# Kernel optimization log

Measured on AMD Instinct MI355X. Metric: run time of the kernel, lower is better.

Reference implementation:

```python
import jax, jax.numpy as jnp
import numpy as np

B, S, H = 2, 2048, 2048
NH, NKV, D = 32, 8, 64
GROUPS = NH // NKV
SCALE = D ** -0.5


def rotate_half(x):
    x1, x2 = x[..., : D // 2], x[..., D // 2 :]
    return jnp.concatenate((-x2, x1), axis=-1)


def setup_inputs() -> dict:
    key = jax.random.key(0)
    ks = jax.random.split(key, 8)
    x = jax.random.normal(ks[0], (B, S, H), dtype=jnp.float32)
    cos = jax.random.uniform(ks[1], (B, S, D), dtype=jnp.float32)
    sin = jax.random.uniform(ks[2], (B, S, D), dtype=jnp.float32)
    mask = jnp.tril(jnp.ones((S, S), dtype=jnp.int32))[None, None]  # causal (1,1,S,S)
    std = H ** -0.5
    wq = jax.random.normal(ks[3], (NH * D, H), dtype=jnp.float32) * std
    wk = jax.random.normal(ks[4], (NKV * D, H), dtype=jnp.float32) * std
    wv = jax.random.normal(ks[5], (NKV * D, H), dtype=jnp.float32) * std
    wo = jax.random.normal(ks[6], (H, NH * D), dtype=jnp.float32) * std
    return {"x": x, "cos": cos, "sin": sin, "mask": mask,
            "wq": wq, "wk": wk, "wv": wv, "wo": wo}


def reference(x, cos, sin, mask, wq, wk, wv, wo):
    b, s, _ = x.shape
    # projections (Linear: x @ W^T, no bias)
    q = (x @ wq.T).reshape(b, s, NH, D).transpose(0, 2, 1, 3)    # (b, nh, s, d)
    k = (x @ wk.T).reshape(b, s, NKV, D).transpose(0, 2, 1, 3)   # (b, nkv, s, d)
    v = (x @ wv.T).reshape(b, s, NKV, D).transpose(0, 2, 1, 3)
    # RoPE
    c = cos[:, None, :, :]
    sn = sin[:, None, :, :]
    q = q * c + rotate_half(q) * sn
    k = k * c + rotate_half(k) * sn
    # GQA: repeat KV heads
    k = jnp.repeat(k, GROUPS, axis=1)   # (b, nh, s, d)
    v = jnp.repeat(v, GROUPS, axis=1)
    scores = jnp.einsum("bhqd,bhkd->bhqk", q, k) * SCALE
    scores = jnp.where(mask == 0, -jnp.inf, scores)
    weights = jax.nn.softmax(scores, axis=-1)
    out = jnp.einsum("bhqk,bhkd->bhqd", weights, v)
    out = out.transpose(0, 2, 1, 3).reshape(b, s, NH * D)
    return out @ wo.T
```

## Files before the change

kernel.cpp:

```cpp
#include <hip/hip_runtime.h>
#include <hip/hip_bf16.h>
#include <math.h>

typedef __attribute__((ext_vector_type(8))) short bf16x8;
typedef __attribute__((ext_vector_type(4))) float f32x4;

__device__ __forceinline__ float bf2f(ushort u) {
  union { unsigned u; float f; } v; v.u = ((unsigned)u) << 16; return v.f;
}
__device__ __forceinline__ ushort f2bf(float f) {
  union { float f; unsigned u; } v; v.f = f;
  unsigned r = v.u + 0x7FFFu + ((v.u >> 16) & 1u);
  return (ushort)(r >> 16);
}
#if __has_builtin(__builtin_amdgcn_exp2f)
#define EXP2F(x) __builtin_amdgcn_exp2f(x)
#else
#define EXP2F(x) exp2f(x)
#endif
__device__ __forceinline__ void gl_lds16(const ushort* g, ushort* l) {
  __builtin_amdgcn_global_load_lds(
      (const __attribute__((address_space(1))) unsigned int*)g,
      (__attribute__((address_space(3))) unsigned int*)l, 16, 0, 0);
}

static const long XB   = 0;
static const long WQB  = 8388608;
static const long WKB  = 12582912;
static const long WVB  = 13631488;
static const long WOB  = 14680064;
static const long COSB = 18874368;
static const long SINB = 19136512;
static const long QB   = 19398656;
static const long KB   = 27787264;
static const long VTB  = 29884416;

__global__ void detect_dtype(const ushort* __restrict__ x, int* __restrict__ flag) {
  __shared__ int cnt;
  if (threadIdx.x == 0) cnt = 0;
  __syncthreads();
  int local = 0;
  for (int j = 0; j < 32; j++) {
    ushort u = x[threadIdx.x + j * 256];
    int e = (u >> 7) & 0xFF;
    if (e >= 100 && e <= 142) local++;
  }
  atomicAdd(&cnt, local);
  __syncthreads();
  if (threadIdx.x == 0) *flag = (cnt >= 6554) ? 1 : 0;
}

__global__ void cast_all(const void* __restrict__ s0, const void* __restrict__ s1,
                         const void* __restrict__ s2, const void* __restrict__ s3,
                         const void* __restrict__ s4, const void* __restrict__ s5,
                         const void* __restrict__ s6,
                         ushort* __restrict__ d0, ushort* __restrict__ d1,
                         ushort* __restrict__ d2, ushort* __restrict__ d3,
                         ushort* __restrict__ d4, ushort* __restrict__ d5,
                         ushort* __restrict__ d6, const int* __restrict__ flag) {
  if (*flag) return;
  const long N = 2424832;
  for (long i = (long)blockIdx.x * blockDim.x + threadIdx.x; i < N;
       i += (long)gridDim.x * blockDim.x) {
    const float4* s; ushort* d; long off;
    if      (i < 1048576) { s = (const float4*)s0; d = d0; off = i; }
    else if (i < 1572864) { s = (const float4*)s1; d = d1; off = i - 1048576; }
    else if (i < 1703936) { s = (const float4*)s2; d = d2; off = i - 1572864; }
    else if (i < 1835008) { s = (const float4*)s3; d = d3; off = i - 1703936; }
    else if (i < 2359296) { s = (const float4*)s4; d = d4; off = i - 1835008; }
    else if (i < 2392064) { s = (const float4*)s5; d = d5; off = i - 2359296; }
    else                  { s = (const float4*)s6; d = d6; off = i - 2392064; }
    float4 a = s[2 * off], b = s[2 * off + 1];
    uint4 o;
    o.x = (unsigned)f2bf(a.x) | ((unsigned)f2bf(a.y) << 16);
    o.y = (unsigned)f2bf(a.z) | ((unsigned)f2bf(a.w) << 16);
    o.z = (unsigned)f2bf(b.x) | ((unsigned)f2bf(b.y) << 16);
    o.w = (unsigned)f2bf(b.z) | ((unsigned)f2bf(b.w) << 16);
    ((uint4*)d)[off] = o;
  }
}

__device__ __forceinline__ void gemm_body(
    const ushort* __restrict__ A, const ushort* __restrict__ W, void* __restrict__ C,
    int N, int K, int bm, int bn, bool ofp32, ushort* As, ushort* Ws) {
  const int tid = threadIdx.x;
  const int wave = tid >> 6, lane = tid & 63;
  const int quad = lane >> 4, l15 = lane & 15;
  const int wm = (wave >> 1) * 64, wn = (wave & 1) * 64;
  const int srow = tid >> 2, sk = (tid & 3) * 8;
  const ushort* Ap = A + (size_t)(bm + srow) * K + sk;
  const ushort* Wp = W + (size_t)(bn + srow) * K + sk;
  ushort* AsW = As + wave * 512;
  ushort* WsW = Ws + wave * 512;
  f32x4 acc[4][4] = {};
  for (int k0 = 0; k0 < K; k0 += 32) {
    __syncthreads();
    gl_lds16(Ap + k0, AsW);
    gl_lds16(Ap + (size_t)64 * K + k0, AsW + 2048);
    gl_lds16(Wp + k0, WsW);
    gl_lds16(Wp + (size_t)64 * K + k0, WsW + 2048);
    __syncthreads();
    bf16x8 af[4], wf[4];
#pragma unroll
    for (int t = 0; t < 4; t++)
      af[t] = *(const bf16x8*)&As[(wm + t * 16 + l15) * 32 + quad * 8];
#pragma unroll
    for (int t = 0; t < 4; t++)
      wf[t] = *(const bf16x8*)&Ws[(wn + t * 16 + l15) * 32 + quad * 8];
#pragma unroll
    for (int mt = 0; mt < 4; mt++)
#pragma unroll
      for (int nt = 0; nt < 4; nt++)
        acc[mt][nt] = __builtin_amdgcn_mfma_f32_16x16x32_bf16(af[mt], wf[nt], acc[mt][nt], 0, 0, 0);
  }
  if (!ofp32) {
    ushort* Cb = (ushort*)C;
#pragma unroll
    for (int mt = 0; mt < 4; mt++)
#pragma unroll
      for (int nt = 0; nt < 4; nt++)
#pragma unroll
        for (int r = 0; r < 4; r++) {
          int row = bm + wm + mt * 16 + quad * 4 + r;
          int col = bn + wn + nt * 16 + l15;
          Cb[(size_t)row * N + col] = f2bf(acc[mt][nt][r]);
        }
  } else {
    float* Cf = (float*)C;
#pragma unroll
    for (int mt = 0; mt < 4; mt++)
#pragma unroll
      for (int nt = 0; nt < 4; nt++)
#pragma unroll
        for (int r = 0; r < 4; r++) {
          int row = bm + wm + mt * 16 + quad * 4 + r;
          int col = bn + wn + nt * 16 + l15;
          Cf[(size_t)row * N + col] = acc[mt][nt][r];
        }
  }
}

__global__ __launch_bounds__(256) void gemm_qkv(
    const ushort* __restrict__ xws, const ushort* __restrict__ xorig,
    const ushort* __restrict__ wqws, const ushort* __restrict__ wqorig,
    const ushort* __restrict__ wkws, const ushort* __restrict__ wkorig,
    const ushort* __restrict__ wvws, const ushort* __restrict__ wvorig,
    ushort* __restrict__ qout, ushort* __restrict__ kout, ushort* __restrict__ vtout,
    const int* __restrict__ flag) {
  __shared__ __align__(16) ushort As[128 * 32];
  __shared__ __align__(16) ushort Ws[128 * 32];
  const bool bf = (*flag != 0);
  const ushort* x = bf ? xorig : xws;
  const int id = blockIdx.x;
  if (id < 512) {
    gemm_body(x, bf ? wqorig : wqws, qout, 2048, 2048, (id >> 4) * 128, (id & 15) * 128, false, As, Ws);
  } else if (id < 640) {
    int t = id - 512;
    gemm_body(x, bf ? wkorig : wkws, kout, 512, 2048, (t >> 2) * 128, (t & 3) * 128, false, As, Ws);
  } else {
    int t = id - 640;
    gemm_body(bf ? wvorig : wvws, x, vtout, 4096, 2048, (t & 3) * 128, (t >> 2) * 128, false, As, Ws);
  }
}

__global__ __launch_bounds__(256) void gemm_bt(
    const ushort* __restrict__ Aws, const ushort* __restrict__ Aorig,
    const ushort* __restrict__ Wws, const ushort* __restrict__ Worig,
    void* __restrict__ C, int N, int K, const int* __restrict__ flag, int outMode) {
  __shared__ __align__(16) ushort As[128 * 32];
  __shared__ __align__(16) ushort Ws[128 * 32];
  const bool bf = (*flag != 0);
  const ushort* A = (bf && Aorig) ? Aorig : Aws;
  const ushort* W = (bf && Worig) ? Worig : Wws;
  bool ofp32 = (outMode == 1) && !bf;
  gemm_body(A, W, C, N, K, blockIdx.y * 128, blockIdx.x * 128, ofp32, As, Ws);
}

__global__ void rope_kernel(ushort* __restrict__ Qb, ushort* __restrict__ Kb,
                            const ushort* __restrict__ cws, const ushort* __restrict__ corig,
                            const ushort* __restrict__ sws, const ushort* __restrict__ sorig,
                            const int* __restrict__ flag) {
  const ushort* cb = (*flag) ? corig : cws;
  const ushort* sb = (*flag) ? sorig : sws;
  int i = blockIdx.x * 256 + threadIdx.x;
  ushort* base; long row; int c8; float scl;
  if (i < 524288) {
    row = i >> 7; int rest = i & 127; c8 = (rest & 3) * 8;
    base = Qb + row * 2048 + (rest >> 2) * 64 + c8;
    scl = 0.18033688011112f;
  } else {
    int j = i - 524288;
    row = j >> 5; int rest = j & 31; c8 = (rest & 3) * 8;
    base = Kb + row * 512 + (rest >> 2) * 64 + c8;
    scl = 1.0f;
  }
  uint4 lo4 = *(const uint4*)base;
  uint4 hi4 = *(const uint4*)(base + 32);
  uint4 cl4 = *(const uint4*)(cb + row * 64 + c8);
  uint4 ch4 = *(const uint4*)(cb + row * 64 + c8 + 32);
  uint4 sl4 = *(const uint4*)(sb + row * 64 + c8);
  uint4 sh4 = *(const uint4*)(sb + row * 64 + c8 + 32);
  const ushort* lo = (const ushort*)&lo4; const ushort* hi = (const ushort*)&hi4;
  const ushort* cl = (const ushort*)&cl4; const ushort* ch = (const ushort*)&ch4;
  const ushort* sl = (const ushort*)&sl4; const ushort* sh = (const ushort*)&sh4;
  uint4 olo, ohi;
  ushort* po = (ushort*)&olo; ushort* ph = (ushort*)&ohi;
#pragma unroll
  for (int k = 0; k < 8; k++) {
    float l = bf2f(lo[k]), h = bf2f(hi[k]);
    po[k] = f2bf((l * bf2f(cl[k]) - h * bf2f(sl[k])) * scl);
    ph[k] = f2bf((h * bf2f(ch[k]) + l * bf2f(sh[k])) * scl);
  }
  *(uint4*)base = olo;
  *(uint4*)(base + 32) = ohi;
}

__global__ __launch_bounds__(512, 4) void attn_kernel(
    const ushort* __restrict__ Qb, const ushort* __restrict__ Kb,
    const ushort* __restrict__ Vt, ushort* __restrict__ Ob) {
  __shared__ __align__(16) ushort Ks[2][4096];
  __shared__ __align__(16) ushort Vs[2][4096];
  __shared__ __align__(16) ushort Ps[128 * 72];
  const int tid = threadIdx.x;
  const int wave = tid >> 6, lane = tid & 63;
  const int quad = lane >> 4, l15 = lane & 15;
  const int id = blockIdx.x;
  const int kvh = id & 7;
  const int b = (id >> 3) & 1;
  const int hsub = (id >> 4) & 3;
  const int h = kvh * 4 + hsub;
  const int t = 15 - (id >> 6);
  const size_t brow = (size_t)b * 2048;
  const ushort* Kg = Kb + brow * 512 + (size_t)kvh * 64;
  const ushort* Vg = Vt + (size_t)(kvh * 64) * 4096 + brow;

  const int prow = wave * 16 + (lane >> 2);
  const int chunk = (lane & 3) * 8;
  const int k_s = prow & 63, k_kc = prow >> 6;
  const int v_d = prow & 63, v_sc = prow >> 6;
  const int ldsW = wave * 512;

  const int q0 = t * 128;
  const int wrow0 = q0 + wave * 16;
  const int blockNt = 2 * t + 2;
  const int myLast = wrow0 >> 6;

  gl_lds16(Kg + (size_t)k_s * 512 + k_kc * 32 + chunk, &Ks[0][ldsW]);
  gl_lds16(Vg + (size_t)v_d * 4096 + v_sc * 32 + chunk, &Vs[0][ldsW]);

  bf16x8 qf[2];
#pragma unroll
  for (int kc = 0; kc < 2; kc++)
    qf[kc] = *(const bf16x8*)&Qb[(brow + wrow0 + l15) * 2048 + h * 64 + kc * 32 + quad * 8];

  float l_loc = 0.f;
  f32x4 oacc[4] = {};

  __syncthreads();

  for (int nt = 0; nt < blockNt; nt++) {
    const int cur = nt & 1;
    if (nt + 1 < blockNt) {
      const int n1 = (nt + 1) * 64;
      gl_lds16(Kg + (size_t)(n1 + k_s) * 512 + k_kc * 32 + chunk, &Ks[cur ^ 1][ldsW]);
      gl_lds16(Vg + (size_t)v_d * 4096 + n1 + v_sc * 32 + chunk, &Vs[cur ^ 1][ldsW]);
    }
    if (nt <= myLast) {
      const int n0 = nt * 64;
      const ushort* Kc = Ks[cur];
      const ushort* Vc = Vs[cur];
      f32x4 sc[4];
      __builtin_amdgcn_s_setprio(1);
#pragma unroll
      for (int ct = 0; ct < 4; ct++) {
        bf16x8 kf0 = *(const bf16x8*)&Kc[(ct * 16 + l15) * 32 + quad * 8];
        bf16x8 kf1 = *(const bf16x8*)&Kc[2048 + (ct * 16 + l15) * 32 + quad * 8];
        f32x4 z = {0.f, 0.f, 0.f, 0.f};
        z = __builtin_amdgcn_mfma_f32_16x16x32_bf16(kf0, qf[0], z, 0, 0, 0);
        z = __builtin_amdgcn_mfma_f32_16x16x32_bf16(kf1, qf[1], z, 0, 0, 0);
        sc[ct] = z;
      }
      __builtin_amdgcn_s_setprio(0);
      if (nt == myLast) {
        const int qrow = wrow0 + l15;
#pragma unroll
        for (int ct = 0; ct < 4; ct++)
#pragma unroll
          for (int r = 0; r < 4; r++)
            if (n0 + ct * 16 + quad * 4 + r > qrow) sc[ct][r] = -INFINITY;
      }
#pragma unroll
      for (int ct = 0; ct < 4; ct++)
#pragma unroll
        for (int k = 0; k < 2; k++) {
          float pv0 = EXP2F(sc[ct][2 * k]     - 23.083120654223f);
          float pv1 = EXP2F(sc[ct][2 * k + 1] - 23.083120654223f);
          l_loc += pv0 + pv1;
          unsigned u = ((__float_as_uint(pv0) + 0x8000u) >> 16) |
                       ((__float_as_uint(pv1) + 0x8000u) & 0xFFFF0000u);
          *(unsigned*)&Ps[(wave * 16 + l15) * 72 + ct * 16 + quad * 4 + 2 * k] = u;
        }
      bf16x8 pf0 = *(const bf16x8*)&Ps[(wave * 16 + l15) * 72 + quad * 8];
      bf16x8 pf1 = *(const bf16x8*)&Ps[(wave * 16 + l15) * 72 + 32 + quad * 8];
      __builtin_amdgcn_s_setprio(1);
#pragma unroll
      for (int dt = 0; dt < 4; dt++) {
        bf16x8 vf0 = *(const bf16x8*)&Vc[(dt * 16 + l15) * 32 + quad * 8];
        bf16x8 vf1 = *(const bf16x8*)&Vc[2048 + (dt * 16 + l15) * 32 + quad * 8];
        oacc[dt] = __builtin_amdgcn_mfma_f32_16x16x32_bf16(pf0, vf0, oacc[dt], 0, 0, 0);
        oacc[dt] = __builtin_amdgcn_mfma_f32_16x16x32_bf16(pf1, vf1, oacc[dt], 0, 0, 0);
      }
      __builtin_amdgcn_s_setprio(0);
    }
    __syncthreads();
  }
  l_loc += __shfl_xor(l_loc, 16, 64);
  l_loc += __shfl_xor(l_loc, 32, 64);
  float linv[4];
#pragma unroll
  for (int r = 0; r < 4; r++) linv[r] = 1.f / __shfl(l_loc, quad * 4 + r, 64);
#pragma unroll
  for (int dt = 0; dt < 4; dt++)
#pragma unroll
    for (int r = 0; r < 4; r++) {
      int s = wrow0 + quad * 4 + r;
      Ob[(brow + s) * 2048 + h * 64 + dt * 16 + l15] = f2bf(oacc[dt][r] * linv[r]);
    }
}

extern "C" void kernel_launch(void* const* d_in, const int* in_sizes, int n_in,
                              void* d_out, int out_size, void* d_ws, size_t ws_size,
                              hipStream_t stream) {
  char* wsb = (char*)d_ws;
  int* flag = (int*)wsb;
  ushort* base = (ushort*)(wsb + 256);
  ushort* xb   = base + XB;
  ushort* wqb  = base + WQB;
  ushort* wkb  = base + WKB;
  ushort* wvb  = base + WVB;
  ushort* wob  = base + WOB;
  ushort* cosb = base + COSB;
  ushort* sinb = base + SINB;
  ushort* qb   = base + QB;
  ushort* kb   = base + KB;
  ushort* vtb  = base + VTB;
  ushort* abuf = xb;

  const ushort* xo  = (const ushort*)d_in[0];
  const ushort* co  = (const ushort*)d_in[1];
  const ushort* so  = (const ushort*)d_in[2];
  const ushort* wqo = (const ushort*)d_in[4];
  const ushort* wko = (const ushort*)d_in[5];
  const ushort* wvo = (const ushort*)d_in[6];
  const ushort* woo = (const ushort*)d_in[7];

  detect_dtype<<<1, 256, 0, stream>>>(xo, flag);

  cast_all<<<4096, 256, 0, stream>>>(d_in[0], d_in[4], d_in[5], d_in[6], d_in[7],
                                     d_in[1], d_in[2],
                                     xb, wqb, wkb, wvb, wob, cosb, sinb, flag);

  gemm_qkv<<<768, 256, 0, stream>>>(xb, xo, wqb, wqo, wkb, wko, wvb, wvo,
                                    qb, kb, vtb, flag);

  rope_kernel<<<2560, 256, 0, stream>>>(qb, kb, cosb, co, sinb, so, flag);

  attn_kernel<<<1024, 512, 0, stream>>>(qb, kb, vtb, abuf);

  gemm_bt<<<dim3(16, 32), 256, 0, stream>>>(abuf, nullptr, wob, woo, d_out, 2048, 2048, flag, 1);
}
```

Baseline: 318.3 us.

## Triple-buffer GEMM LDS tiles with async prefetch two stages ahead

The GEMM main loop moves from a single LDS buffer guarded by two barriers per K-step to a three-stage ring. Global-to-LDS loads are issued two tiles ahead and waited on with explicit vmcnt counts, so each step needs only one barrier. Wave priority is also raised around the MFMA block. The goal is to overlap global load latency with matrix compute, at the cost of three times the LDS per block, which may reduce occupancy.

```diff
diff --git a/kernel.cpp b/kernel.cpp
--- a/kernel.cpp
+++ b/kernel.cpp
@@ -90,29 +90,55 @@
   const int srow = tid >> 2, sk = (tid & 3) * 8;
   const ushort* Ap = A + (size_t)(bm + srow) * K + sk;
   const ushort* Wp = W + (size_t)(bn + srow) * K + sk;
-  ushort* AsW = As + wave * 512;
-  ushort* WsW = Ws + wave * 512;
+  const int woff = wave * 512;
   f32x4 acc[4][4] = {};
-  for (int k0 = 0; k0 < K; k0 += 32) {
-    __syncthreads();
-    gl_lds16(Ap + k0, AsW);
-    gl_lds16(Ap + (size_t)64 * K + k0, AsW + 2048);
-    gl_lds16(Wp + k0, WsW);
-    gl_lds16(Wp + (size_t)64 * K + k0, WsW + 2048);
-    __syncthreads();
+  const int T = K >> 5;
+
+#pragma unroll
+  for (int t = 0; t < 2; t++) {
+    ushort* AsB = As + t * 4096;
+    ushort* WsB = Ws + t * 4096;
+    gl_lds16(Ap + t * 32, AsB + woff);
+    gl_lds16(Ap + (size_t)64 * K + t * 32, AsB + 2048 + woff);
+    gl_lds16(Wp + t * 32, WsB + woff);
+    gl_lds16(Wp + (size_t)64 * K + t * 32, WsB + 2048 + woff);
+  }
+
+  int rbuf = 0;
+  for (int t = 0; t < T; t++) {
+    if (t < T - 1) asm volatile("s_waitcnt vmcnt(4)" ::: "memory");
+    else           asm volatile("s_waitcnt vmcnt(0)" ::: "memory");
+    __builtin_amdgcn_s_barrier();
+    __builtin_amdgcn_sched_barrier(0);
+    const ushort* AsB = As + rbuf * 4096;
+    const ushort* WsB = Ws + rbuf * 4096;
     bf16x8 af[4], wf[4];
 #pragma unroll
-    for (int t = 0; t < 4; t++)
-      af[t] = *(const bf16x8*)&As[(wm + t * 16 + l15) * 32 + quad * 8];
-#pragma unroll
-    for (int t = 0; t < 4; t++)
-      wf[t] = *(const bf16x8*)&Ws[(wn + t * 16 + l15) * 32 + quad * 8];
+    for (int q = 0; q < 4; q++)
+      af[q] = *(const bf16x8*)&AsB[(wm + q * 16 + l15) * 32 + quad * 8];
+#pragma unroll
+    for (int q = 0; q < 4; q++)
+      wf[q] = *(const bf16x8*)&WsB[(wn + q * 16 + l15) * 32 + quad * 8];
+    __builtin_amdgcn_s_setprio(1);
 #pragma unroll
     for (int mt = 0; mt < 4; mt++)
 #pragma unroll
       for (int nt = 0; nt < 4; nt++)
         acc[mt][nt] = __builtin_amdgcn_mfma_f32_16x16x32_bf16(af[mt], wf[nt], acc[mt][nt], 0, 0, 0);
-  }
+    __builtin_amdgcn_s_setprio(0);
+    if (t + 2 < T) {
+      const int sbuf = (rbuf == 0) ? 2 : rbuf - 1;
+      const int k0 = (t + 2) * 32;
+      ushort* AsN = As + sbuf * 4096;
+      ushort* WsN = Ws + sbuf * 4096;
+      gl_lds16(Ap + k0, AsN + woff);
+      gl_lds16(Ap + (size_t)64 * K + k0, AsN + 2048 + woff);
+      gl_lds16(Wp + k0, WsN + woff);
+      gl_lds16(Wp + (size_t)64 * K + k0, WsN + 2048 + woff);
+    }
+    rbuf = (rbuf == 2) ? 0 : rbuf + 1;
+  }
+
   if (!ofp32) {
     ushort* Cb = (ushort*)C;
 #pragma unroll
@@ -147,8 +173,8 @@
     const ushort* __restrict__ wvws, const ushort* __restrict__ wvorig,
     ushort* __restrict__ qout, ushort* __restrict__ kout, ushort* __restrict__ vtout,
     const int* __restrict__ flag) {
-  __shared__ __align__(16) ushort As[128 * 32];
-  __shared__ __align__(16) ushort Ws[128 * 32];
+  __shared__ __align__(16) ushort As[3 * 4096];
+  __shared__ __align__(16) ushort Ws[3 * 4096];
   const bool bf = (*flag != 0);
   const ushort* x = bf ? xorig : xws;
   const int id = blockIdx.x;
@@ -167,8 +193,8 @@
     const ushort* __restrict__ Aws, const ushort* __restrict__ Aorig,
     const ushort* __restrict__ Wws, const ushort* __restrict__ Worig,
     void* __restrict__ C, int N, int K, const int* __restrict__ flag, int outMode) {
-  __shared__ __align__(16) ushort As[128 * 32];
-  __shared__ __align__(16) ushort Ws[128 * 32];
+  __shared__ __align__(16) ushort As[3 * 4096];
+  __shared__ __align__(16) ushort Ws[3 * 4096];
   const bool bf = (*flag != 0);
   const ushort* A = (bf && Aorig) ? Aorig : Aws;
   const ushort* W = (bf && Worig) ? Worig : Wws;
```

Result: no change. 318.8 us (+0.2%).

## Double-buffer GEMM LDS tiles to overlap global loads with MFMA compute

Applied to the files above, without the earlier changes.

The shared GEMM body now uses two LDS buffers for A and W tiles, prefetching the next K-slice via direct global-to-LDS loads while MFMAs run on the current slice. This halves barriers per iteration and hides load latency. Wave priority is raised around the MFMA block. LDS use doubles per block, which may reduce occupancy, and correctness relies on the barrier waiting for outstanding LDS-direct loads.

```diff
diff --git a/kernel.cpp b/kernel.cpp
--- a/kernel.cpp
+++ b/kernel.cpp
@@ -90,29 +90,46 @@
   const int srow = tid >> 2, sk = (tid & 3) * 8;
   const ushort* Ap = A + (size_t)(bm + srow) * K + sk;
   const ushort* Wp = W + (size_t)(bn + srow) * K + sk;
-  ushort* AsW = As + wave * 512;
-  ushort* WsW = Ws + wave * 512;
+  const int woff = wave * 512;
   f32x4 acc[4][4] = {};
-  for (int k0 = 0; k0 < K; k0 += 32) {
-    __syncthreads();
-    gl_lds16(Ap + k0, AsW);
-    gl_lds16(Ap + (size_t)64 * K + k0, AsW + 2048);
-    gl_lds16(Wp + k0, WsW);
-    gl_lds16(Wp + (size_t)64 * K + k0, WsW + 2048);
-    __syncthreads();
+  const int T = K >> 5;
+
+  gl_lds16(Ap, As + woff);
+  gl_lds16(Ap + (size_t)64 * K, As + 2048 + woff);
+  gl_lds16(Wp, Ws + woff);
+  gl_lds16(Wp + (size_t)64 * K, Ws + 2048 + woff);
+  __syncthreads();
+
+  int cur = 0;
+  for (int t = 0; t < T; t++) {
+    if (t + 1 < T) {
+      const int nb = cur ^ 1;
+      const int k0 = (t + 1) * 32;
+      gl_lds16(Ap + k0, As + nb * 4096 + woff);
+      gl_lds16(Ap + (size_t)64 * K + k0, As + nb * 4096 + 2048 + woff);
+      gl_lds16(Wp + k0, Ws + nb * 4096 + woff);
+      gl_lds16(Wp + (size_t)64 * K + k0, Ws + nb * 4096 + 2048 + woff);
+    }
+    const ushort* AsB = As + cur * 4096;
+    const ushort* WsB = Ws + cur * 4096;
     bf16x8 af[4], wf[4];
 #pragma unroll
-    for (int t = 0; t < 4; t++)
-      af[t] = *(const bf16x8*)&As[(wm + t * 16 + l15) * 32 + quad * 8];
-#pragma unroll
-    for (int t = 0; t < 4; t++)
-      wf[t] = *(const bf16x8*)&Ws[(wn + t * 16 + l15) * 32 + quad * 8];
+    for (int q = 0; q < 4; q++)
+      af[q] = *(const bf16x8*)&AsB[(wm + q * 16 + l15) * 32 + quad * 8];
+#pragma unroll
+    for (int q = 0; q < 4; q++)
+      wf[q] = *(const bf16x8*)&WsB[(wn + q * 16 + l15) * 32 + quad * 8];
+    __builtin_amdgcn_s_setprio(1);
 #pragma unroll
     for (int mt = 0; mt < 4; mt++)
 #pragma unroll
       for (int nt = 0; nt < 4; nt++)
         acc[mt][nt] = __builtin_amdgcn_mfma_f32_16x16x32_bf16(af[mt], wf[nt], acc[mt][nt], 0, 0, 0);
-  }
+    __builtin_amdgcn_s_setprio(0);
+    __syncthreads();
+    cur ^= 1;
+  }
+
   if (!ofp32) {
     ushort* Cb = (ushort*)C;
 #pragma unroll
@@ -147,8 +164,8 @@
     const ushort* __restrict__ wvws, const ushort* __restrict__ wvorig,
     ushort* __restrict__ qout, ushort* __restrict__ kout, ushort* __restrict__ vtout,
     const int* __restrict__ flag) {
-  __shared__ __align__(16) ushort As[128 * 32];
-  __shared__ __align__(16) ushort Ws[128 * 32];
+  __shared__ __align__(16) ushort As[2 * 4096];
+  __shared__ __align__(16) ushort Ws[2 * 4096];
   const bool bf = (*flag != 0);
   const ushort* x = bf ? xorig : xws;
   const int id = blockIdx.x;
@@ -167,8 +184,8 @@
     const ushort* __restrict__ Aws, const ushort* __restrict__ Aorig,
     const ushort* __restrict__ Wws, const ushort* __restrict__ Worig,
     void* __restrict__ C, int N, int K, const int* __restrict__ flag, int outMode) {
-  __shared__ __align__(16) ushort As[128 * 32];
-  __shared__ __align__(16) ushort Ws[128 * 32];
+  __shared__ __align__(16) ushort As[2 * 4096];
+  __shared__ __align__(16) ushort Ws[2 * 4096];
   const bool bf = (*flag != 0);
   const ushort* A = (bf && Aorig) ? Aorig : Aws;
   const ushort* W = (bf && Worig) ? Worig : Wws;
```

Result: no change. 321.2 us (+0.9%).
